# Kernel optimization log

Hardware: AMD Instinct MI355X
Metric: run time of the kernel (lower is better)

The kernel has to match this reference:

```python
import jax, jax.numpy as jnp
import numpy as np

N_NODES = 25000
N_EDGES = 400000
IN_DIM, HID_DIM, OUT_DIM = 174, 128, 64


def setup_inputs() -> dict:
    key = jax.random.key(0)
    ks = jax.random.split(key, 8)
    x = jax.random.normal(ks[0], (N_NODES, IN_DIM), dtype=jnp.float32)
    edge_index = jax.random.randint(ks[1], (2, N_EDGES), 0, N_NODES, dtype=jnp.int64)
    # PyG SAGEConv params: lin_l (neighbors, with bias), lin_r (root, no bias)
    def glorot(k, shape):
        lim = float(np.sqrt(6.0 / (shape[0] + shape[1])))
        return jax.random.uniform(k, shape, jnp.float32, -lim, lim)
    W1_l = glorot(ks[2], (HID_DIM, IN_DIM))
    W1_r = glorot(ks[3], (HID_DIM, IN_DIM))
    b1 = jnp.zeros((HID_DIM,), jnp.float32)
    W2_l = glorot(ks[4], (OUT_DIM, HID_DIM))
    W2_r = glorot(ks[5], (OUT_DIM, HID_DIM))
    b2 = jnp.zeros((OUT_DIM,), jnp.float32)
    return {"x": x, "edge_index": edge_index, "W1_l": W1_l, "b1": b1,
            "W1_r": W1_r, "W2_l": W2_l, "b2": b2, "W2_r": W2_r}


def _sage_conv(h, src, dst, W_l, b, W_r):
    # mean-aggregate neighbor features at destination nodes
    msg = h[src]                                       # [E, F] gather
    summed = jax.ops.segment_sum(msg, dst, num_segments=N_NODES)  # [N, F]
    deg = jax.ops.segment_sum(jnp.ones((src.shape[0],), h.dtype), dst,
                              num_segments=N_NODES)    # [N]
    mean = summed / jnp.maximum(deg, 1.0)[:, None]
    # out = lin_l(mean) + lin_r(h)
    return mean @ W_l.T + b + h @ W_r.T


def reference(x, edge_index, W1_l, b1, W1_r, W2_l, b2, W2_r):
    src, dst = edge_index[0], edge_index[1]
    h = _sage_conv(x, src, dst, W1_l, b1, W1_r)
    h = jax.nn.relu(h)
    # dropout is identity in eval mode (module exposes freeze() for inference)
    out = _sage_conv(h, src, dst, W2_l, b2, W2_r)
    return out
```

## Files before the change

### kernel.cpp

```cpp
#include <hip/hip_runtime.h>

#define N_NODES 25000
#define N_EDGES 400000
#define IN_DIM 174
#define HID_DIM 128
#define OUT_DIM 64
#define MPAD 25088
#define BINCAP 64

using u32 = unsigned int;
typedef __attribute__((ext_vector_type(8))) short s16x8;
typedef __attribute__((ext_vector_type(4))) float f32x4;
typedef __attribute__((ext_vector_type(4))) u32 u32x4;

__device__ __forceinline__ float bflo(u32 u) { u32 t = u << 16; return __builtin_bit_cast(float, t); }
__device__ __forceinline__ float bfhi(u32 u) { u32 t = u & 0xffff0000u; return __builtin_bit_cast(float, t); }
__device__ __forceinline__ u32 f2b(float f) {
    u32 u = __builtin_bit_cast(u32, f);
    return (u + 0x7fffu + ((u >> 16) & 1u)) >> 16;
}
__device__ __forceinline__ u32 packbf2(float a, float b) { return f2b(a) | (f2b(b) << 16); }

__device__ __forceinline__ void gload_lds16(const void* g, void* l) {
    __builtin_amdgcn_global_load_lds(
        (const __attribute__((address_space(1))) u32*)g,
        (__attribute__((address_space(3))) u32*)l, 16, 0, 0);
}

#define WB1_CNT (256 * 96)
#define WB2_CNT (128 * 64)
#define PREP_TOT (WB1_CNT + WB2_CNT + N_NODES)

__global__ __launch_bounds__(256) void prep_w_kernel(
    const float* __restrict__ W1l, const float* __restrict__ W1r,
    const float* __restrict__ W2l, const float* __restrict__ W2r,
    u32* __restrict__ wb1, u32* __restrict__ wb2, int* __restrict__ degI) {
    int idx = blockIdx.x * blockDim.x + threadIdx.x;
    if (idx < WB1_CNT) {
        int nrow = idx / 96, d2 = idx - nrow * 96;
        const float* src = (nrow < 128) ? W1l + (size_t)nrow * IN_DIM
                                        : W1r + (size_t)(nrow - 128) * IN_DIM;
        float2 v = make_float2(0.f, 0.f);
        if (d2 < 87) v = ((const float2*)src)[d2];
        wb1[idx] = packbf2(v.x, v.y);
        return;
    }
    idx -= WB1_CNT;
    if (idx < WB2_CNT) {
        int nrow = idx >> 6, d2 = idx & 63;
        const float* src = (nrow < 64) ? W2l + (size_t)nrow * HID_DIM
                                       : W2r + (size_t)(nrow - 64) * HID_DIM;
        float2 v = ((const float2*)src)[d2];
        wb2[idx] = packbf2(v.x, v.y);
        return;
    }
    idx -= WB2_CNT;
    if (idx < N_NODES) degI[idx] = 0;
}

#define G1_GEMM_BLOCKS 392
#define G1_EDGE_BLOCKS ((N_EDGES / 4 + 255) / 256)

__global__ __launch_bounds__(256) void gemm1_fused_kernel(
    const float* __restrict__ x, const ushort* __restrict__ wb1,
    ushort* __restrict__ y1n, ushort* __restrict__ y1r,
    const int* __restrict__ ei, int* __restrict__ degI, int* __restrict__ bins) {
    const int bid = blockIdx.x;
    const int tid = threadIdx.x;

    if (bid >= G1_GEMM_BLOCKS) {
        int e4 = ((bid - G1_GEMM_BLOCKS) * 256 + tid) * 4;
        if (e4 < N_EDGES) {
            int4 s = *(const int4*)(ei + e4);
            int4 t = *(const int4*)(ei + N_EDGES + e4);
            int p0 = atomicAdd(&degI[t.x], 1);
            if (p0 < BINCAP) bins[t.x * BINCAP + p0] = s.x;
            int p1 = atomicAdd(&degI[t.y], 1);
            if (p1 < BINCAP) bins[t.y * BINCAP + p1] = s.y;
            int p2 = atomicAdd(&degI[t.z], 1);
            if (p2 < BINCAP) bins[t.z * BINCAP + p2] = s.z;
            int p3 = atomicAdd(&degI[t.w], 1);
            if (p3 < BINCAP) bins[t.w * BINCAP + p3] = s.w;
        }
        return;
    }

    __shared__ ushort As[64 * 32];
    __shared__ ushort Bs[256 * 32];
    const int lane = tid & 63, w = tid >> 6;
    const int m0 = bid * 64;
    const int wmo = (w >> 1) * 32;
    const int wno = (w & 1) * 128;
    const int arow = lane >> 2;
    const int achunk = (lane & 3) * 8;
    const int r4 = tid >> 2;
    const int q  = tid & 3;
    const int fr = lane & 15, fo = (lane >> 4) * 8;
    const bool mfull = (bid < 390);

    f32x4 acc[2][8] = {};

    for (int kk = 0; kk < 192; kk += 32) {
        #pragma unroll
        for (int c = 0; c < 4; ++c) {
            int r = w * 64 + c * 16;
            gload_lds16(wb1 + (size_t)(r + arow) * 192 + kk + achunk, &Bs[r * 32]);
        }
        {
            int gm = m0 + r4;
            u32x4 o;
            if (mfull || gm < N_NODES) {
                const float* xr = x + (size_t)gm * IN_DIM + kk + q * 8;
                if (kk < 160) {
                    #pragma unroll
                    for (int e = 0; e < 4; ++e) {
                        float2 v = ((const float2*)xr)[e];
                        o[e] = packbf2(v.x, v.y);
                    }
                } else {
                    #pragma unroll
                    for (int e = 0; e < 4; ++e) {
                        int col = kk + q * 8 + e * 2;
                        float2 v = make_float2(0.f, 0.f);
                        if (col < IN_DIM) v = ((const float2*)xr)[e];
                        o[e] = packbf2(v.x, v.y);
                    }
                }
            } else {
                o[0] = 0u; o[1] = 0u; o[2] = 0u; o[3] = 0u;
            }
            ((u32x4*)As)[r4 * 4 + q] = o;
        }
        __syncthreads();
        s16x8 af[2], bf[8];
        #pragma unroll
        for (int i = 0; i < 2; ++i)
            af[i] = *(const s16x8*)&As[(wmo + i * 16 + fr) * 32 + fo];
        #pragma unroll
        for (int j = 0; j < 8; ++j)
            bf[j] = *(const s16x8*)&Bs[(wno + j * 16 + fr) * 32 + fo];
        #pragma unroll
        for (int i = 0; i < 2; ++i)
            #pragma unroll
            for (int j = 0; j < 8; ++j)
                acc[i][j] = __builtin_amdgcn_mfma_f32_16x16x32_bf16(af[i], bf[j], acc[i][j], 0, 0, 0);
        __syncthreads();
    }

    const int cr = (lane >> 4) * 4, cc = lane & 15;
    #pragma unroll
    for (int i = 0; i < 2; ++i)
        #pragma unroll
        for (int r = 0; r < 4; ++r) {
            int row = m0 + wmo + i * 16 + cr + r;
            #pragma unroll
            for (int j = 0; j < 8; ++j) {
                int colg = wno + j * 16 + cc;
                ushort* Cp = (colg < 128) ? y1n : y1r;
                int c = colg & 127;
                Cp[(size_t)row * 128 + c] = (ushort)f2b(acc[i][j][r]);
            }
        }
}

__global__ __launch_bounds__(256) void gemm2_kernel(
    const ushort* __restrict__ h1, const ushort* __restrict__ wb2,
    ushort* __restrict__ y2n, ushort* __restrict__ y2r) {
    __shared__ ushort As[64 * 32];
    __shared__ ushort Bs[128 * 32];
    const int tid = threadIdx.x;
    const int lane = tid & 63, w = tid >> 6;
    const int m0 = blockIdx.x * 64;
    const int wmo = (w >> 1) * 32, wno = (w & 1) * 64;
    const int arow = lane >> 2;
    const int achunk = (lane & 3) * 8;
    const int fr = lane & 15, fo = (lane >> 4) * 8;

    f32x4 acc[2][4] = {};

    for (int kk = 0; kk < 128; kk += 32) {
        {
            int r = w * 16;
            gload_lds16(h1 + (size_t)(m0 + r + arow) * 128 + kk + achunk, &As[r * 32]);
        }
        #pragma unroll
        for (int c = 0; c < 2; ++c) {
            int r = w * 32 + c * 16;
            gload_lds16(wb2 + (size_t)(r + arow) * 128 + kk + achunk, &Bs[r * 32]);
        }
        __syncthreads();
        s16x8 af[2], bf[4];
        #pragma unroll
        for (int i = 0; i < 2; ++i)
            af[i] = *(const s16x8*)&As[(wmo + i * 16 + fr) * 32 + fo];
        #pragma unroll
        for (int j = 0; j < 4; ++j)
            bf[j] = *(const s16x8*)&Bs[(wno + j * 16 + fr) * 32 + fo];
        #pragma unroll
        for (int i = 0; i < 2; ++i)
            #pragma unroll
            for (int j = 0; j < 4; ++j)
                acc[i][j] = __builtin_amdgcn_mfma_f32_16x16x32_bf16(af[i], bf[j], acc[i][j], 0, 0, 0);
        __syncthreads();
    }

    const int cr = (lane >> 4) * 4, cc = lane & 15;
    #pragma unroll
    for (int i = 0; i < 2; ++i)
        #pragma unroll
        for (int r = 0; r < 4; ++r) {
            int row = m0 + wmo + i * 16 + cr + r;
            #pragma unroll
            for (int j = 0; j < 4; ++j) {
                int colg = wno + j * 16 + cc;
                ushort* Cp = (colg < 64) ? y2n : y2r;
                int c = colg & 63;
                Cp[(size_t)row * 64 + c] = (ushort)f2b(acc[i][j][r]);
            }
        }
}

__global__ __launch_bounds__(256) void agg1_kernel(const u32* __restrict__ y1n,
                                                   const u32* __restrict__ y1r,
                                                   const int* __restrict__ degI,
                                                   const int* __restrict__ bins,
                                                   const float* __restrict__ b1,
                                                   u32* __restrict__ h1) {
    int w = threadIdx.x >> 6, lane = threadIdx.x & 63;
    int n = blockIdx.x * 4 + w;
    if (n >= N_NODES) return;
    int deg = degI[n];
    int d = min(deg, BINCAP);
    const int* bp = bins + n * BINCAP;
    float a0 = 0.f, a1 = 0.f;
    int j = 0;
    for (; j + 16 <= d; j += 16) {
        int4 sa = *(const int4*)(bp + j);
        int4 sb = *(const int4*)(bp + j + 4);
        int4 sc = *(const int4*)(bp + j + 8);
        int4 sd = *(const int4*)(bp + j + 12);
        u32 u0 = y1n[(size_t)sa.x * 64 + lane];
        u32 u1 = y1n[(size_t)sa.y * 64 + lane];
        u32 u2 = y1n[(size_t)sa.z * 64 + lane];
        u32 u3 = y1n[(size_t)sa.w * 64 + lane];
        u32 u4 = y1n[(size_t)sb.x * 64 + lane];
        u32 u5 = y1n[(size_t)sb.y * 64 + lane];
        u32 u6 = y1n[(size_t)sb.z * 64 + lane];
        u32 u7 = y1n[(size_t)sb.w * 64 + lane];
        u32 u8 = y1n[(size_t)sc.x * 64 + lane];
        u32 u9 = y1n[(size_t)sc.y * 64 + lane];
        u32 ua = y1n[(size_t)sc.z * 64 + lane];
        u32 ub = y1n[(size_t)sc.w * 64 + lane];
        u32 uc = y1n[(size_t)sd.x * 64 + lane];
        u32 ud = y1n[(size_t)sd.y * 64 + lane];
        u32 ue = y1n[(size_t)sd.z * 64 + lane];
        u32 uf = y1n[(size_t)sd.w * 64 + lane];
        a0 += bflo(u0) + bflo(u1) + bflo(u2) + bflo(u3)
            + bflo(u4) + bflo(u5) + bflo(u6) + bflo(u7)
            + bflo(u8) + bflo(u9) + bflo(ua) + bflo(ub)
            + bflo(uc) + bflo(ud) + bflo(ue) + bflo(uf);
        a1 += bfhi(u0) + bfhi(u1) + bfhi(u2) + bfhi(u3)
            + bfhi(u4) + bfhi(u5) + bfhi(u6) + bfhi(u7)
            + bfhi(u8) + bfhi(u9) + bfhi(ua) + bfhi(ub)
            + bfhi(uc) + bfhi(ud) + bfhi(ue) + bfhi(uf);
    }
    if (j + 8 <= d) {
        int4 sa = *(const int4*)(bp + j);
        int4 sb = *(const int4*)(bp + j + 4);
        u32 u0 = y1n[(size_t)sa.x * 64 + lane];
        u32 u1 = y1n[(size_t)sa.y * 64 + lane];
        u32 u2 = y1n[(size_t)sa.z * 64 + lane];
        u32 u3 = y1n[(size_t)sa.w * 64 + lane];
        u32 u4 = y1n[(size_t)sb.x * 64 + lane];
        u32 u5 = y1n[(size_t)sb.y * 64 + lane];
        u32 u6 = y1n[(size_t)sb.z * 64 + lane];
        u32 u7 = y1n[(size_t)sb.w * 64 + lane];
        a0 += bflo(u0) + bflo(u1) + bflo(u2) + bflo(u3)
            + bflo(u4) + bflo(u5) + bflo(u6) + bflo(u7);
        a1 += bfhi(u0) + bfhi(u1) + bfhi(u2) + bfhi(u3)
            + bfhi(u4) + bfhi(u5) + bfhi(u6) + bfhi(u7);
        j += 8;
    }
    if (j + 4 <= d) {
        int4 s4 = *(const int4*)(bp + j);
        u32 u0 = y1n[(size_t)s4.x * 64 + lane];
        u32 u1 = y1n[(size_t)s4.y * 64 + lane];
        u32 u2 = y1n[(size_t)s4.z * 64 + lane];
        u32 u3 = y1n[(size_t)s4.w * 64 + lane];
        a0 += bflo(u0) + bflo(u1) + bflo(u2) + bflo(u3);
        a1 += bfhi(u0) + bfhi(u1) + bfhi(u2) + bfhi(u3);
        j += 4;
    }
    for (; j < d; ++j) {
        int s = bp[j];
        u32 u = y1n[(size_t)s * 64 + lane];
        a0 += bflo(u); a1 += bfhi(u);
    }
    float inv = 1.f / fmaxf((float)deg, 1.f);
    u32 ur = y1r[(size_t)n * 64 + lane];
    float2 bb = ((const float2*)b1)[lane];
    float v0 = fmaxf(a0 * inv + bflo(ur) + bb.x, 0.f);
    float v1 = fmaxf(a1 * inv + bfhi(ur) + bb.y, 0.f);
    h1[(size_t)n * 64 + lane] = packbf2(v0, v1);
}

__global__ __launch_bounds__(256) void agg2_kernel(const u32* __restrict__ y2n,
                                                   const u32* __restrict__ y2r,
                                                   const int* __restrict__ degI,
                                                   const int* __restrict__ bins,
                                                   const float* __restrict__ b2,
                                                   float2* __restrict__ out) {
    int w = threadIdx.x >> 6, lane = threadIdx.x & 63;
    int half = lane >> 5, dd = lane & 31;
    int n = blockIdx.x * 4 + w;
    if (n >= N_NODES) return;
    int deg = degI[n];
    int d = min(deg, BINCAP);
    const int* bp = bins + n * BINCAP;
    float a0 = 0.f, a1 = 0.f;
    int j = 0;
    for (; j + 16 <= d; j += 16) {
        int s0 = bp[j + half],      s1 = bp[j + 2 + half];
        int s2 = bp[j + 4 + half],  s3 = bp[j + 6 + half];
        int s4 = bp[j + 8 + half],  s5 = bp[j + 10 + half];
        int s6 = bp[j + 12 + half], s7 = bp[j + 14 + half];
        u32 u0 = y2n[(size_t)s0 * 32 + dd];
        u32 u1 = y2n[(size_t)s1 * 32 + dd];
        u32 u2 = y2n[(size_t)s2 * 32 + dd];
        u32 u3 = y2n[(size_t)s3 * 32 + dd];
        u32 u4 = y2n[(size_t)s4 * 32 + dd];
        u32 u5 = y2n[(size_t)s5 * 32 + dd];
        u32 u6 = y2n[(size_t)s6 * 32 + dd];
        u32 u7 = y2n[(size_t)s7 * 32 + dd];
        a0 += bflo(u0) + bflo(u1) + bflo(u2) + bflo(u3)
            + bflo(u4) + bflo(u5) + bflo(u6) + bflo(u7);
        a1 += bfhi(u0) + bfhi(u1) + bfhi(u2) + bfhi(u3)
            + bfhi(u4) + bfhi(u5) + bfhi(u6) + bfhi(u7);
    }
    if (j + 8 <= d) {
        int s0 = bp[j + half],     s1 = bp[j + 2 + half];
        int s2 = bp[j + 4 + half], s3 = bp[j + 6 + half];
        u32 u0 = y2n[(size_t)s0 * 32 + dd];
        u32 u1 = y2n[(size_t)s1 * 32 + dd];
        u32 u2 = y2n[(size_t)s2 * 32 + dd];
        u32 u3 = y2n[(size_t)s3 * 32 + dd];
        a0 += bflo(u0) + bflo(u1) + bflo(u2) + bflo(u3);
        a1 += bfhi(u0) + bfhi(u1) + bfhi(u2) + bfhi(u3);
        j += 8;
    }
    if (j + 4 <= d) {
        int s0 = bp[j + half], s1 = bp[j + 2 + half];
        u32 u0 = y2n[(size_t)s0 * 32 + dd];
        u32 u1 = y2n[(size_t)s1 * 32 + dd];
        a0 += bflo(u0) + bflo(u1);
        a1 += bfhi(u0) + bfhi(u1);
        j += 4;
    }
    if (j + 2 <= d) {
        int s = bp[j + half];
        u32 u = y2n[(size_t)s * 32 + dd];
        a0 += bflo(u); a1 += bfhi(u);
        j += 2;
    }
    if (j < d && half == 0) {
        int s = bp[j];
        u32 u = y2n[(size_t)s * 32 + dd];
        a0 += bflo(u); a1 += bfhi(u);
    }
    a0 += __shfl_xor(a0, 32, 64);
    a1 += __shfl_xor(a1, 32, 64);
    if (half == 0) {
        float inv = 1.f / fmaxf((float)deg, 1.f);
        u32 ur = y2r[(size_t)n * 32 + dd];
        float2 bb = ((const float2*)b2)[dd];
        float2 o;
        o.x = a0 * inv + bflo(ur) + bb.x;
        o.y = a1 * inv + bfhi(ur) + bb.y;
        out[(size_t)n * 32 + dd] = o;
    }
}


extern "C" void kernel_launch(void* const* d_in, const int* in_sizes, int n_in,
                              void* d_out, int out_size, void* d_ws, size_t ws_size,
                              hipStream_t stream) {
    const float* x   = (const float*)d_in[0];
    const int*   ei  = (const int*)d_in[1];
    const float* W1l = (const float*)d_in[2];
    const float* b1  = (const float*)d_in[3];
    const float* W1r = (const float*)d_in[4];
    const float* W2l = (const float*)d_in[5];
    const float* b2  = (const float*)d_in[6];
    const float* W2r = (const float*)d_in[7];

    char* wp = (char*)d_ws;
    auto alloc = [&](size_t bytes) -> char* {
        char* p = wp;
        wp += (bytes + 255) & ~(size_t)255;
        return p;
    };
    int* degI = (int*)alloc((size_t)N_NODES * 4);
    int* bins = (int*)alloc((size_t)N_NODES * BINCAP * 4);
    u32* wb1  = (u32*)alloc((size_t)WB1_CNT * 4);
    u32* wb2  = (u32*)alloc((size_t)WB2_CNT * 4);
    u32* y1n  = (u32*)alloc((size_t)MPAD * 64 * 4);
    u32* y1r  = (u32*)alloc((size_t)MPAD * 64 * 4);
    u32* h1   = (u32*)alloc((size_t)MPAD * 64 * 4);
    u32* y2n  = (u32*)alloc((size_t)MPAD * 32 * 4);
    u32* y2r  = (u32*)alloc((size_t)MPAD * 32 * 4);

    prep_w_kernel<<<(PREP_TOT + 255) / 256, 256, 0, stream>>>(
        W1l, W1r, W2l, W2r, wb1, wb2, degI);
    gemm1_fused_kernel<<<G1_GEMM_BLOCKS + G1_EDGE_BLOCKS, 256, 0, stream>>>(
        x, (const ushort*)wb1, (ushort*)y1n, (ushort*)y1r, ei, degI, bins);
    agg1_kernel<<<(N_NODES + 3) / 4, 256, 0, stream>>>(
        y1n, y1r, degI, bins, b1, h1);
    gemm2_kernel<<<392, 256, 0, stream>>>(
        (const ushort*)h1, (const ushort*)wb2, (ushort*)y2n, (ushort*)y2r);
    agg2_kernel<<<(N_NODES + 3) / 4, 256, 0, stream>>>(
        y2n, y2r, degI, bins, b2, (float2*)d_out);
}
```

Measured before the change: 73.94 us.

## Enlarge gemm1 M-tile to 128 rows and remap agg2 to quarter-wave per node

gemm1 now processes 128 rows per block instead of 64, halving the number of GEMM blocks and reusing each loaded weight tile across twice as many rows, at the cost of more accumulators and registers per thread. agg2 now assigns 16 lanes per node, and each lane loads 8-byte vectors covering four features, so a wave handles four nodes. This removes the half-wave split and the shuffle reduction and writes float4 outputs. Fewer GEMM blocks may leave compute units underused, and the register growth may lower occupancy.

Result: slower. 79.00 us (+6.8%).

```diff
diff --git a/kernel.cpp b/kernel.cpp
--- a/kernel.cpp
+++ b/kernel.cpp
@@ -12,6 +12,7 @@
 typedef __attribute__((ext_vector_type(8))) short s16x8;
 typedef __attribute__((ext_vector_type(4))) float f32x4;
 typedef __attribute__((ext_vector_type(4))) u32 u32x4;
+typedef __attribute__((ext_vector_type(2))) u32 u32x2;
 
 __device__ __forceinline__ float bflo(u32 u) { u32 t = u << 16; return __builtin_bit_cast(float, t); }
 __device__ __forceinline__ float bfhi(u32 u) { u32 t = u & 0xffff0000u; return __builtin_bit_cast(float, t); }
@@ -58,7 +59,7 @@
     if (idx < N_NODES) degI[idx] = 0;
 }
 
-#define G1_GEMM_BLOCKS 392
+#define G1_GEMM_BLOCKS 196
 #define G1_EDGE_BLOCKS ((N_EDGES / 4 + 255) / 256)
 
 __global__ __launch_bounds__(256) void gemm1_fused_kernel(
@@ -85,20 +86,20 @@
         return;
     }
 
-    __shared__ ushort As[64 * 32];
+    __shared__ ushort As[128 * 32];
     __shared__ ushort Bs[256 * 32];
     const int lane = tid & 63, w = tid >> 6;
-    const int m0 = bid * 64;
-    const int wmo = (w >> 1) * 32;
+    const int m0 = bid * 128;
+    const int wmo = (w >> 1) * 64;
     const int wno = (w & 1) * 128;
     const int arow = lane >> 2;
     const int achunk = (lane & 3) * 8;
     const int r4 = tid >> 2;
     const int q  = tid & 3;
     const int fr = lane & 15, fo = (lane >> 4) * 8;
-    const bool mfull = (bid < 390);
-
-    f32x4 acc[2][8] = {};
+    const bool mfull = (bid < 195);
+
+    f32x4 acc[4][8] = {};
 
     for (int kk = 0; kk < 192; kk += 32) {
         #pragma unroll
@@ -106,8 +107,10 @@
             int r = w * 64 + c * 16;
             gload_lds16(wb1 + (size_t)(r + arow) * 192 + kk + achunk, &Bs[r * 32]);
         }
-        {
-            int gm = m0 + r4;
+        #pragma unroll
+        for (int it = 0; it < 2; ++it) {
+            int r = it * 64 + r4;
+            int gm = m0 + r;
             u32x4 o;
             if (mfull || gm < N_NODES) {
                 const float* xr = x + (size_t)gm * IN_DIM + kk + q * 8;
@@ -129,18 +132,18 @@
             } else {
                 o[0] = 0u; o[1] = 0u; o[2] = 0u; o[3] = 0u;
             }
-            ((u32x4*)As)[r4 * 4 + q] = o;
+            ((u32x4*)As)[r * 4 + q] = o;
         }
         __syncthreads();
-        s16x8 af[2], bf[8];
-        #pragma unroll
-        for (int i = 0; i < 2; ++i)
+        s16x8 af[4], bf[8];
+        #pragma unroll
+        for (int i = 0; i < 4; ++i)
             af[i] = *(const s16x8*)&As[(wmo + i * 16 + fr) * 32 + fo];
         #pragma unroll
         for (int j = 0; j < 8; ++j)
             bf[j] = *(const s16x8*)&Bs[(wno + j * 16 + fr) * 32 + fo];
         #pragma unroll
-        for (int i = 0; i < 2; ++i)
+        for (int i = 0; i < 4; ++i)
             #pragma unroll
             for (int j = 0; j < 8; ++j)
                 acc[i][j] = __builtin_amdgcn_mfma_f32_16x16x32_bf16(af[i], bf[j], acc[i][j], 0, 0, 0);
@@ -149,7 +152,7 @@
 
     const int cr = (lane >> 4) * 4, cc = lane & 15;
     #pragma unroll
-    for (int i = 0; i < 2; ++i)
+    for (int i = 0; i < 4; ++i)
         #pragma unroll
         for (int r = 0; r < 4; ++r) {
             int row = m0 + wmo + i * 16 + cr + r;
@@ -304,80 +307,56 @@
     h1[(size_t)n * 64 + lane] = packbf2(v0, v1);
 }
 
+#define A2LD(s) { u32x2 v = *(const u32x2*)(y2n + (size_t)(s) * 32 + 2 * l); \
+    a0 += bflo(v.x); a1 += bfhi(v.x); a2 += bflo(v.y); a3 += bfhi(v.y); }
+
 __global__ __launch_bounds__(256) void agg2_kernel(const u32* __restrict__ y2n,
                                                    const u32* __restrict__ y2r,
                                                    const int* __restrict__ degI,
                                                    const int* __restrict__ bins,
                                                    const float* __restrict__ b2,
-                                                   float2* __restrict__ out) {
+                                                   float* __restrict__ out) {
     int w = threadIdx.x >> 6, lane = threadIdx.x & 63;
-    int half = lane >> 5, dd = lane & 31;
-    int n = blockIdx.x * 4 + w;
+    int q = lane >> 4, l = lane & 15;
+    int n = blockIdx.x * 16 + w * 4 + q;
     if (n >= N_NODES) return;
     int deg = degI[n];
     int d = min(deg, BINCAP);
     const int* bp = bins + n * BINCAP;
-    float a0 = 0.f, a1 = 0.f;
+    float a0 = 0.f, a1 = 0.f, a2 = 0.f, a3 = 0.f;
     int j = 0;
     for (; j + 16 <= d; j += 16) {
-        int s0 = bp[j + half],      s1 = bp[j + 2 + half];
-        int s2 = bp[j + 4 + half],  s3 = bp[j + 6 + half];
-        int s4 = bp[j + 8 + half],  s5 = bp[j + 10 + half];
-        int s6 = bp[j + 12 + half], s7 = bp[j + 14 + half];
-        u32 u0 = y2n[(size_t)s0 * 32 + dd];
-        u32 u1 = y2n[(size_t)s1 * 32 + dd];
-        u32 u2 = y2n[(size_t)s2 * 32 + dd];
-        u32 u3 = y2n[(size_t)s3 * 32 + dd];
-        u32 u4 = y2n[(size_t)s4 * 32 + dd];
-        u32 u5 = y2n[(size_t)s5 * 32 + dd];
-        u32 u6 = y2n[(size_t)s6 * 32 + dd];
-        u32 u7 = y2n[(size_t)s7 * 32 + dd];
-        a0 += bflo(u0) + bflo(u1) + bflo(u2) + bflo(u3)
-            + bflo(u4) + bflo(u5) + bflo(u6) + bflo(u7);
-        a1 += bfhi(u0) + bfhi(u1) + bfhi(u2) + bfhi(u3)
-            + bfhi(u4) + bfhi(u5) + bfhi(u6) + bfhi(u7);
+        int s0 = bp[j + 0],  s1 = bp[j + 1],  s2 = bp[j + 2],  s3 = bp[j + 3];
+        int s4 = bp[j + 4],  s5 = bp[j + 5],  s6 = bp[j + 6],  s7 = bp[j + 7];
+        int s8 = bp[j + 8],  s9 = bp[j + 9],  sa = bp[j + 10], sb = bp[j + 11];
+        int sc = bp[j + 12], sd = bp[j + 13], se = bp[j + 14], sf = bp[j + 15];
+        A2LD(s0) A2LD(s1) A2LD(s2) A2LD(s3) A2LD(s4) A2LD(s5) A2LD(s6) A2LD(s7)
+        A2LD(s8) A2LD(s9) A2LD(sa) A2LD(sb) A2LD(sc) A2LD(sd) A2LD(se) A2LD(sf)
     }
     if (j + 8 <= d) {
-        int s0 = bp[j + half],     s1 = bp[j + 2 + half];
-        int s2 = bp[j + 4 + half], s3 = bp[j + 6 + half];
-        u32 u0 = y2n[(size_t)s0 * 32 + dd];
-        u32 u1 = y2n[(size_t)s1 * 32 + dd];
-        u32 u2 = y2n[(size_t)s2 * 32 + dd];
-        u32 u3 = y2n[(size_t)s3 * 32 + dd];
-        a0 += bflo(u0) + bflo(u1) + bflo(u2) + bflo(u3);
-        a1 += bfhi(u0) + bfhi(u1) + bfhi(u2) + bfhi(u3);
+        int s0 = bp[j + 0], s1 = bp[j + 1], s2 = bp[j + 2], s3 = bp[j + 3];
+        int s4 = bp[j + 4], s5 = bp[j + 5], s6 = bp[j + 6], s7 = bp[j + 7];
+        A2LD(s0) A2LD(s1) A2LD(s2) A2LD(s3) A2LD(s4) A2LD(s5) A2LD(s6) A2LD(s7)
         j += 8;
     }
     if (j + 4 <= d) {
-        int s0 = bp[j + half], s1 = bp[j + 2 + half];
-        u32 u0 = y2n[(size_t)s0 * 32 + dd];
-        u32 u1 = y2n[(size_t)s1 * 32 + dd];
-        a0 += bflo(u0) + bflo(u1);
-        a1 += bfhi(u0) + bfhi(u1);
+        int s0 = bp[j + 0], s1 = bp[j + 1], s2 = bp[j + 2], s3 = bp[j + 3];
+        A2LD(s0) A2LD(s1) A2LD(s2) A2LD(s3)
         j += 4;
     }
-    if (j + 2 <= d) {
-        int s = bp[j + half];
-        u32 u = y2n[(size_t)s * 32 + dd];
-        a0 += bflo(u); a1 += bfhi(u);
-        j += 2;
-    }
-    if (j < d && half == 0) {
-        int s = bp[j];
-        u32 u = y2n[(size_t)s * 32 + dd];
-        a0 += bflo(u); a1 += bfhi(u);
-    }
-    a0 += __shfl_xor(a0, 32, 64);
-    a1 += __shfl_xor(a1, 32, 64);
-    if (half == 0) {
-        float inv = 1.f / fmaxf((float)deg, 1.f);
-        u32 ur = y2r[(size_t)n * 32 + dd];
-        float2 bb = ((const float2*)b2)[dd];
-        float2 o;
-        o.x = a0 * inv + bflo(ur) + bb.x;
-        o.y = a1 * inv + bfhi(ur) + bb.y;
-        out[(size_t)n * 32 + dd] = o;
-    }
+    for (; j < d; ++j) {
+        int s0 = bp[j];
+        A2LD(s0)
+    }
+    float inv = 1.f / fmaxf((float)deg, 1.f);
+    u32x2 ur = *(const u32x2*)(y2r + (size_t)n * 32 + 2 * l);
+    float4 bb = ((const float4*)b2)[l];
+    float4 o;
+    o.x = a0 * inv + bflo(ur.x) + bb.x;
+    o.y = a1 * inv + bfhi(ur.x) + bb.y;
+    o.z = a2 * inv + bflo(ur.y) + bb.z;
+    o.w = a3 * inv + bfhi(ur.y) + bb.w;
+    ((float4*)out)[(size_t)n * 16 + l] = o;
 }
 
 
@@ -417,6 +396,6 @@
         y1n, y1r, degI, bins, b1, h1);
     gemm2_kernel<<<392, 256, 0, stream>>>(
         (const ushort*)h1, (const ushort*)wb2, (ushort*)y2n, (ushort*)y2r);
-    agg2_kernel<<<(N_NODES + 3) / 4, 256, 0, stream>>>(
-        y2n, y2r, degI, bins, b2, (float2*)d_out);
-}
+    agg2_kernel<<<(N_NODES + 15) / 16, 256, 0, stream>>>(
+        y2n, y2r, degI, bins, b2, (float*)d_out);
+}
```
